# Optimization experiments

Hardware: AMD Instinct MI355X
Metric: run time of the kernel (lower is better)

Reference implementation:

```python
import jax, jax.numpy as jnp
import numpy as np

B, N = 2, 4096
SA, DG, ED, OUT = 128, 1024, 4, 128
RF = 0.1   # ED_radius_factor
EPS = 1e-5  # BatchNorm eps


def setup_inputs() -> dict:
    key = jax.random.key(0)
    ks = jax.random.split(key, 16)
    def w(k, sh, sc=0.05):
        return jax.random.normal(k, sh, jnp.float32) * sc
    return dict(
        pointcloud=jax.random.normal(ks[0], (B, N, 3), jnp.float32),
        h1=jax.random.normal(ks[1], (B, SA, N), jnp.float32),
        h2=jax.random.normal(ks[2], (B, DG, N), jnp.float32),
        dg_w1=w(ks[3], (256, DG)), dg_b1=jnp.zeros(256), dg_g1=jnp.ones(256), dg_be1=jnp.zeros(256),
        dg_w2=w(ks[4], (64, 256)), dg_b2=jnp.zeros(64), dg_g2=jnp.ones(64), dg_be2=jnp.zeros(64),
        dg_w3=w(ks[5], (32, 64)), dg_b3=jnp.zeros(32), dg_g3=jnp.ones(32), dg_be3=jnp.zeros(32),
        ed_w1=w(ks[6], (3, ED), 0.5), ed_b1=jnp.zeros(ED),
        ed_w2=w(ks[7], (ED, ED), 0.5), ed_b2=jnp.zeros(ED),
        w1=w(ks[8], (512, SA + 32 + ED)), b1=jnp.zeros(512), g1=jnp.ones(512), be1=jnp.zeros(512),
        w2=w(ks[9], (256, 512)), b2=jnp.zeros(256), g2=jnp.ones(256), be2=jnp.zeros(256),
        w3=w(ks[10], (OUT, 256)), b3=jnp.zeros(OUT), g3=jnp.ones(OUT), be3=jnp.zeros(OUT),
    )


def _conv1x1(x, w, b):  # x: (B,C,N) 1x1 Conv1d
    return jnp.einsum('oc,bcn->bon', w, x) + b[None, :, None]


def _bn(x, g, b):  # training-mode BatchNorm1d over (B,N) per channel
    m = x.mean(axis=(0, 2), keepdims=True)
    v = ((x - m) ** 2).mean(axis=(0, 2), keepdims=True)
    return g[None, :, None] * (x - m) * jax.lax.rsqrt(v + EPS) + b[None, :, None]


def _eigs(xyz):  # (N,3) -> (N,3) eigenvalues of per-point radius-neighbor covariance
    n = xyz.shape[0]
    x2 = (xyz * xyz).sum(-1)
    d2 = jnp.maximum(x2[:, None] + x2[None, :] - 2.0 * (xyz @ xyz.T), 0.0)
    dist = jnp.sqrt(jnp.maximum(d2, 1e-12))
    eye = jnp.eye(n, dtype=bool)
    max_d = jnp.where(eye, -jnp.inf, dist).max()  # calculate_distances max
    radius = max_d * RF                            # adaptive radius
    mask = ((dist < radius) & ~eye).astype(xyz.dtype)  # (N,N) radius neighbors, no self
    cnt = mask.sum(1)                              # true neighbor count (for the mean)
    mu = (mask @ xyz) / jnp.maximum(cnt, 1.0)[:, None]
    # sum_j m_ij x_j x_j^T via one matmul on flattened outer products
    S = (mask @ (xyz[:, :, None] * xyz[:, None, :]).reshape(n, 9)).reshape(n, 3, 3)
    # NOTE: original divides by k = mask.shape[0] == N (not neighbor count) -- kept faithfully
    cov = (S - cnt[:, None, None] * mu[:, :, None] * mu[:, None, :]) / n
    return jnp.linalg.eigvalsh(cov)


def reference(pointcloud, h1, h2,
              dg_w1, dg_b1, dg_g1, dg_be1,
              dg_w2, dg_b2, dg_g2, dg_be2,
              dg_w3, dg_b3, dg_g3, dg_be3,
              ed_w1, ed_b1, ed_w2, ed_b2,
              w1, b1, g1, be1, w2, b2, g2, be2, w3, b3, g3, be3):
    xyz = pointcloud[..., 0:3]
    # DG head: 1024 -> 256 -> 64 -> 32 (1x1 conv + BN + ReLU)
    f2 = jax.nn.relu(_bn(_conv1x1(h2, dg_w1, dg_b1), dg_g1, dg_be1))
    f2 = jax.nn.relu(_bn(_conv1x1(f2, dg_w2, dg_b2), dg_g2, dg_be2))
    f2 = jax.nn.relu(_bn(_conv1x1(f2, dg_w3, dg_b3), dg_g3, dg_be3))
    # ED branch: per-point local PCA eigenvalues + tiny MLP (3->4->4)
    eig = jax.vmap(_eigs)(xyz)                        # (B,N,3)
    h3 = jax.nn.relu(eig @ ed_w1 + ed_b1) @ ed_w2 + ed_b2  # (B,N,4)
    z = jnp.concatenate([h1, f2, jnp.transpose(h3, (0, 2, 1))], axis=1)  # (B,164,N)
    z = jax.nn.relu(_bn(_conv1x1(z, w1, b1), g1, be1))
    z = jax.nn.relu(_bn(_conv1x1(z, w2, b2), g2, be2))
    z = jax.nn.relu(_bn(_conv1x1(z, w3, b3), g3, be3))
    return (xyz, z)
```

## Files before the change

### kernel.cpp

```cpp
#include <hip/hip_runtime.h>
#include <math.h>

#define NPTS 4096
#define NB 2
#define BIGNEG -3.0e38f

typedef __attribute__((ext_vector_type(8))) short short8;
typedef __attribute__((ext_vector_type(4))) float f32x4;
typedef unsigned int uint32;

__device__ __forceinline__ unsigned short f2bf(float f) {
  uint32 u = __float_as_uint(f);
  uint32 r = (u + 0x7FFFu + ((u >> 16) & 1u)) >> 16;
  return (unsigned short)r;
}
__device__ __forceinline__ uint2 pack4(float a, float b, float c, float d) {
  uint2 r;
  r.x = (uint32)f2bf(a) | ((uint32)f2bf(b) << 16);
  r.y = (uint32)f2bf(c) | ((uint32)f2bf(d) << 16);
  return r;
}
__device__ __forceinline__ float bflo(uint32 w) { return __uint_as_float((w & 0xffffu) << 16); }
__device__ __forceinline__ float bfhi(uint32 w) { return __uint_as_float(w & 0xffff0000u); }

struct PrepP {
  const float *h2, *h1, *pc;
  const float* wsrc[6];
  unsigned short* wdst[6];
  unsigned short *h2t, *Zt;
  float *aZ, *bZ, *fZ, *f0;
  unsigned int* mx;
};

union ShPrep {
  float tile[64][65];
  struct { float4 sp[512]; float lm[8]; } m;
};

__global__ __launch_bounds__(256)
void prep_maxd2(PrepP P) {
  __shared__ ShPrep sh;
  int bid = blockIdx.x, tid = threadIdx.x;
  if (bid < 2304) {
    const float* src; unsigned short* dst; int S, C, b, c0, n0;
    if (bid < 2048) {
      b = bid >> 10; int r = bid & 1023;
      c0 = (r & 15) * 64; n0 = (r >> 4) * 64;
      src = P.h2; dst = P.h2t; S = 1024; C = 1024;
    } else {
      int r = bid - 2048; b = r >> 7; int r2 = r & 127;
      c0 = (r2 & 1) * 64; n0 = (r2 >> 1) * 64;
      src = P.h1; dst = P.Zt; S = 192; C = 128;
    }
    const float* sb = src + (size_t)b * C * NPTS;
#pragma unroll
    for (int p = 0; p < 4; ++p) {
      int r = (tid >> 4) + p * 16, q = tid & 15;
      float4 v = *(const float4*)(sb + (size_t)(c0 + r) * NPTS + n0 + q * 4);
      sh.tile[r][q * 4 + 0] = v.x;
      sh.tile[r][q * 4 + 1] = v.y;
      sh.tile[r][q * 4 + 2] = v.z;
      sh.tile[r][q * 4 + 3] = v.w;
    }
    __syncthreads();
#pragma unroll
    for (int p = 0; p < 2; ++p) {
      int n = (tid >> 3) + p * 32, j = tid & 7;
      uint2 lo = pack4(sh.tile[j * 8 + 0][n], sh.tile[j * 8 + 1][n], sh.tile[j * 8 + 2][n],
                       sh.tile[j * 8 + 3][n]);
      uint2 hi = pack4(sh.tile[j * 8 + 4][n], sh.tile[j * 8 + 5][n], sh.tile[j * 8 + 6][n],
                       sh.tile[j * 8 + 7][n]);
      *(uint4*)(dst + ((size_t)b * NPTS + n0 + n) * S + c0 + j * 8) =
          make_uint4(lo.x, lo.y, hi.x, hi.y);
    }
  } else if (bid < 2336) {
    int r = bid - 2304;
    for (int idx = r * 256 + tid; idx < NB * NPTS * 7; idx += 32 * 256) {
      int u = idx % 7, n = (idx / 7) & (NPTS - 1), b = idx / (7 * NPTS);
      *(uint2*)(P.Zt + ((size_t)b * NPTS + n) * 192 + 164 + u * 4) = make_uint2(0u, 0u);
    }
  } else if (bid < 2592) {
    const int segKp[6] = {1024, 256, 64, 192, 512, 256};
    const int segM[6] = {256, 64, 32, 512, 256, 128};
    const int segK[6] = {1024, 256, 64, 164, 512, 256};
    const int segEnd[6] = {262144, 278528, 282624, 380928, 512000, 544768};
    int r = bid - 2336;
    for (int idx = r * 256 + tid; idx < 544768; idx += 256 * 256) {
      int w = 0, start = 0;
#pragma unroll
      for (int s = 0; s < 6; ++s)
        if (idx >= segEnd[s]) { w = s + 1; start = segEnd[s]; }
      int local = idx - start, Kp = segKp[w], m = local / Kp, k = local % Kp;
      float v = (m < segM[w] && k < segK[w]) ? P.wsrc[w][m * segK[w] + k] : 0.f;
      P.wdst[w][local] = f2bf(v);
    }
  } else if (bid == 2592) {
    for (int ch = tid; ch < 512; ch += 256) {
      P.f0[ch] = 0.f;
      if (ch < 192) { P.aZ[ch] = 1.f; P.bZ[ch] = 0.f; P.fZ[ch] = BIGNEG; }
    }
  } else {
    int vb = bid - 2593;
    int b = vb >> 9, rem = vb & 511, it = rem & 63, jt = rem >> 6;
    int i0 = it * 64, j0 = jt * 512;
    const float* pb = P.pc + (size_t)b * NPTS * 3;
    for (int t = tid; t < 512; t += 256) {
      int j = j0 + t;
      float x = pb[j * 3], y = pb[j * 3 + 1], z = pb[j * 3 + 2];
      sh.m.sp[t] = make_float4(x, y, z, fmaf(x, x, fmaf(y, y, z * z)));
    }
    __syncthreads();
    int il = tid & 63, sl = tid >> 6;
    int i = i0 + il;
    float xi = pb[i * 3], yi = pb[i * 3 + 1], zi = pb[i * 3 + 2];
    float x2i = fmaf(xi, xi, fmaf(yi, yi, zi * zi));
    float m = 0.f;
#pragma unroll 4
    for (int j = sl * 128, e2 = sl * 128 + 128; j < e2; ++j) {
      float4 pj = sh.m.sp[j];
      float dot = fmaf(xi, pj.x, fmaf(yi, pj.y, zi * pj.z));
      m = fmaxf(m, fmaf(-2.f, dot, x2i + pj.w));
    }
#pragma unroll
    for (int off = 32; off > 0; off >>= 1) m = fmaxf(m, __shfl_xor(m, off, 64));
    if ((tid & 63) == 0) sh.m.lm[tid >> 6] = m;
    __syncthreads();
    if (tid == 0) {
      float v = fmaxf(fmaxf(sh.m.lm[0], sh.m.lm[1]), fmaxf(sh.m.lm[2], sh.m.lm[3]));
      atomicMax(&P.mx[b], __float_as_uint(v));
    }
  }
}

__global__ __launch_bounds__(256)
void eigs_partial(const float* __restrict__ pc, const unsigned int* __restrict__ mx,
                  float* __restrict__ part) {
  __shared__ float4 sp[1024];
  __shared__ float red[4][32][10];
  int b = blockIdx.z, js = blockIdx.y, it = blockIdx.x;
  int i0 = it * 32, j0 = js * 1024;
  int tid = threadIdx.x;
  const float* pb = pc + (size_t)b * NPTS * 3;
  for (int t = tid; t < 1024; t += 256) {
    int j = j0 + t;
    float x = pb[j * 3], y = pb[j * 3 + 1], z = pb[j * 3 + 2];
    sp[t] = make_float4(x, y, z, fmaf(x, x, fmaf(y, y, z * z)));
  }
  __syncthreads();
  int il = tid & 31, sl = tid >> 5;
  int i = i0 + il;
  float xi = pb[i * 3], yi = pb[i * 3 + 1], zi = pb[i * 3 + 2];
  float x2i = fmaf(xi, xi, fmaf(yi, yi, zi * zi));
  float r2 = 0.01f * fmaxf(__uint_as_float(mx[b]), 1e-12f);
  float v0 = 0, v1 = 0, v2 = 0, v3 = 0, v4 = 0, v5 = 0, v6 = 0, v7 = 0, v8 = 0, v9 = 0;
#pragma unroll 2
  for (int j = sl * 128, e2 = sl * 128 + 128; j < e2; ++j) {
    float4 pj = sp[j];
    float dot = fmaf(xi, pj.x, fmaf(yi, pj.y, zi * pj.z));
    float d2 = fmaf(-2.f, dot, x2i + pj.w);
    float msk = d2 < r2 ? 1.f : 0.f;
    float qx = msk * pj.x, qy = msk * pj.y, qz = msk * pj.z;
    v0 += msk; v1 += qx; v2 += qy; v3 += qz;
    v4 = fmaf(qx, pj.x, v4); v5 = fmaf(qx, pj.y, v5); v6 = fmaf(qx, pj.z, v6);
    v7 = fmaf(qy, pj.y, v7); v8 = fmaf(qy, pj.z, v8); v9 = fmaf(qz, pj.z, v9);
  }
  int iloc = i - j0;
  if (iloc >= sl * 128 && iloc < sl * 128 + 128) {
    v0 -= 1.f; v1 -= xi; v2 -= yi; v3 -= zi;
    v4 = fmaf(-xi, xi, v4); v5 = fmaf(-xi, yi, v5); v6 = fmaf(-xi, zi, v6);
    v7 = fmaf(-yi, yi, v7); v8 = fmaf(-yi, zi, v8); v9 = fmaf(-zi, zi, v9);
  }
  float vals[10] = {v0, v1, v2, v3, v4, v5, v6, v7, v8, v9};
#pragma unroll
  for (int v = 0; v < 10; ++v) vals[v] += __shfl_xor(vals[v], 32, 64);
  int w = tid >> 6;
  if ((tid & 63) < 32)
#pragma unroll
    for (int v = 0; v < 10; ++v) red[w][il][v] = vals[v];
  __syncthreads();
  if (tid < 32) {
    int ii = i0 + tid;
    size_t base = ((size_t)(b * 4 + js) * 10) * NPTS + ii;
#pragma unroll
    for (int v = 0; v < 10; ++v)
      part[base + (size_t)v * NPTS] =
          red[0][tid][v] + red[1][tid][v] + red[2][tid][v] + red[3][tid][v];
  }
}

struct GemmP {
  const unsigned short* Wp;
  const unsigned short* X;
  const float *aIn, *bIn, *fIn;
  unsigned short* Y;
  int Ystride;
  float *psum, *psq;
  int M, Kp;
};

template <int BN_IN>
__global__ __launch_bounds__(256)
void gemm_k(GemmP P) {
  __shared__ char db[2][18432];
  __shared__ float ash[512], bsh[512], fsh[512];
  const int tid = threadIdx.x;
  const int b = blockIdx.z, nt = blockIdx.x, mt = blockIdx.y;
  const int n0 = nt * 128, m0 = mt * 64;
  const int lane = tid & 63, wid = tid >> 6;
  const int wm = wid >> 1, wn = wid & 1, g = lane >> 4, c = lane & 15;
  const int kt = P.Kp >> 6;
  const unsigned short* Xb = P.X + (size_t)b * NPTS * P.Kp;

  if (BN_IN) {
    for (int ch = tid; ch < P.Kp; ch += 256) {
      ash[ch] = P.aIn[ch];
      bsh[ch] = P.bIn[ch];
      fsh[ch] = P.fIn[ch];
    }
    __syncthreads();
  }

  uint4 R0[4], R1[4];
  auto loadG = [&](int t, uint4* R) {
    int k0 = t << 6;
#pragma unroll
    for (int i = 0; i < 4; ++i) {
      int u = tid + i * 256, n = u >> 3, s = u & 7;
      R[i] = *(const uint4*)(Xb + (size_t)(n0 + n) * P.Kp + k0 + s * 8);
    }
  };
  auto writeS = [&](int buf, int t, uint4* R) {
    int k0 = t << 6;
#pragma unroll
    for (int i = 0; i < 4; ++i) {
      int u = tid + i * 256, s = u & 7;
      uint4 v = R[i];
      if (BN_IN) {
        int k = k0 + s * 8;
        float4 a0 = *(const float4*)&ash[k], a1 = *(const float4*)&ash[k + 4];
        float4 b0 = *(const float4*)&bsh[k], b1 = *(const float4*)&bsh[k + 4];
        float4 f0 = *(const float4*)&fsh[k], f1 = *(const float4*)&fsh[k + 4];
        uint2 lo = pack4(fmaxf(fmaf(bflo(v.x), a0.x, b0.x), f0.x),
                         fmaxf(fmaf(bfhi(v.x), a0.y, b0.y), f0.y),
                         fmaxf(fmaf(bflo(v.y), a0.z, b0.z), f0.z),
                         fmaxf(fmaf(bfhi(v.y), a0.w, b0.w), f0.w));
        uint2 hi = pack4(fmaxf(fmaf(bflo(v.z), a1.x, b1.x), f1.x),
                         fmaxf(fmaf(bfhi(v.z), a1.y, b1.y), f1.y),
                         fmaxf(fmaf(bflo(v.w), a1.z, b1.z), f1.z),
                         fmaxf(fmaf(bfhi(v.w), a1.w, b1.w), f1.w));
        v = make_uint4(lo.x, lo.y, hi.x, hi.y);
      }
      *(uint4*)&db[buf][(u >> 3) * 144 + (u & 7) * 16] = v;
    }
  };
  auto loadA = [&](int t, uint4* Af) {
    const unsigned short* base = P.Wp + (size_t)(m0 + wm * 32 + c) * P.Kp + (t << 6) + g * 8;
#pragma unroll
    for (int mf = 0; mf < 2; ++mf)
#pragma unroll
      for (int kw = 0; kw < 2; ++kw)
        Af[mf * 2 + kw] = *(const uint4*)(base + (size_t)mf * 16 * P.Kp + kw * 32);
  };

  f32x4 acc[2][4] = {};
  uint4 Acur[4], Anext[4] = {};
  loadG(0, R0);
  loadA(0, Acur);
  writeS(0, 0, R0);
  if (kt > 1) loadG(1, R1);
  __syncthreads();
  int cur = 0;

  auto step = [&](int t, uint4* Rload, uint4* Rwrite) {
    if (t + 2 < kt) loadG(t + 2, Rload);
    if (t + 1 < kt) loadA(t + 1, Anext);
#pragma unroll
    for (int kw = 0; kw < 2; ++kw) {
      union { uint4 u; short8 s; } a0, a1;
      a0.u = Acur[0 * 2 + kw];
      a1.u = Acur[1 * 2 + kw];
#pragma unroll
      for (int nf = 0; nf < 4; ++nf) {
        union { uint4 u; short8 s; } bf;
        bf.u = *(const uint4*)&db[cur][(wn * 64 + nf * 16 + c) * 144 + kw * 64 + g * 16];
        acc[0][nf] = __builtin_amdgcn_mfma_f32_16x16x32_bf16(a0.s, bf.s, acc[0][nf], 0, 0, 0);
        acc[1][nf] = __builtin_amdgcn_mfma_f32_16x16x32_bf16(a1.s, bf.s, acc[1][nf], 0, 0, 0);
      }
    }
    if (t + 1 < kt) writeS(cur ^ 1, t + 1, Rwrite);
    __syncthreads();
    cur ^= 1;
#pragma unroll
    for (int i = 0; i < 4; ++i) Acur[i] = Anext[i];
  };
  for (int t = 0; t < kt;) {
    step(t, R0, R1);
    ++t;
    if (t >= kt) break;
    step(t, R1, R0);
    ++t;
  }

#pragma unroll
  for (int nf = 0; nf < 4; ++nf) {
    int n = n0 + wn * 64 + nf * 16 + c;
    unsigned short* yrow = P.Y + ((size_t)b * NPTS + n) * P.Ystride;
#pragma unroll
    for (int mf = 0; mf < 2; ++mf) {
      int mb = m0 + wm * 32 + mf * 16 + g * 4;
      if (mb < P.M)
        *(uint2*)(yrow + mb) =
            pack4(acc[mf][nf][0], acc[mf][nf][1], acc[mf][nf][2], acc[mf][nf][3]);
    }
  }
  int slot = b * 64 + nt * 2 + wn;
#pragma unroll
  for (int mf = 0; mf < 2; ++mf)
#pragma unroll
    for (int r = 0; r < 4; ++r) {
      float s = 0.f, q = 0.f;
#pragma unroll
      for (int nf = 0; nf < 4; ++nf) {
        float v = acc[mf][nf][r];
        s += v;
        q = fmaf(v, v, q);
      }
#pragma unroll
      for (int m = 1; m < 16; m <<= 1) {
        s += __shfl_xor(s, m, 64);
        q += __shfl_xor(q, m, 64);
      }
      int row = m0 + wm * 32 + mf * 16 + g * 4 + r;
      if (c == 0 && row < P.M) {
        P.psum[(size_t)row * 128 + slot] = s;
        P.psq[(size_t)row * 128 + slot] = q;
      }
    }
}

__global__ __launch_bounds__(128)
void bn_finalize(const float* __restrict__ psum, const float* __restrict__ psq,
                 const float* __restrict__ gamma, const float* __restrict__ beta,
                 float* __restrict__ a_, float* __restrict__ b_, float* __restrict__ f_) {
  int ch = blockIdx.x, t = threadIdx.x;
  float s = psum[(size_t)ch * 128 + t];
  float q = psq[(size_t)ch * 128 + t];
#pragma unroll
  for (int m = 1; m < 64; m <<= 1) {
    s += __shfl_xor(s, m, 64);
    q += __shfl_xor(q, m, 64);
  }
  __shared__ float ws[2][2];
  if ((t & 63) == 0) { ws[t >> 6][0] = s; ws[t >> 6][1] = q; }
  __syncthreads();
  if (t == 0) {
    float S = ws[0][0] + ws[1][0];
    float Q = ws[0][1] + ws[1][1];
    const float inv = 1.f / (float)(NB * NPTS);
    float mean = S * inv;
    float var = fmaxf(Q * inv - mean * mean, 0.f);
    float aa = rsqrtf(var + 1e-5f) * gamma[ch];
    a_[ch] = aa;
    b_[ch] = beta[ch] - mean * aa;
    if (f_) f_[ch] = 0.f;
  }
}

__global__ __launch_bounds__(256)
void eigs_finalize(const float* __restrict__ part, const float* __restrict__ ew1,
                   const float* __restrict__ eb1, const float* __restrict__ ew2,
                   const float* __restrict__ eb2, unsigned short* __restrict__ Zt) {
  int p = blockIdx.x * 256 + threadIdx.x;
  int b = p >> 12, i = p & (NPTS - 1);
  float t[10];
#pragma unroll
  for (int v = 0; v < 10; ++v) {
    float s = 0.f;
#pragma unroll
    for (int js = 0; js < 4; ++js) s += part[((size_t)(b * 4 + js) * 10 + v) * NPTS + i];
    t[v] = s;
  }
  double cntd = (double)t[0];
  double denom = cntd > 1.0 ? cntd : 1.0;
  double mux = t[1] / denom, muy = t[2] / denom, muz = t[3] / denom;
  const double inv_n = 1.0 / (double)NPTS;
  double a00 = ((double)t[4] - cntd * mux * mux) * inv_n;
  double a01 = ((double)t[5] - cntd * mux * muy) * inv_n;
  double a02 = ((double)t[6] - cntd * mux * muz) * inv_n;
  double a11 = ((double)t[7] - cntd * muy * muy) * inv_n;
  double a12 = ((double)t[8] - cntd * muy * muz) * inv_n;
  double a22 = ((double)t[9] - cntd * muz * muz) * inv_n;
  double e0, e1, e2;
  double p1 = a01 * a01 + a02 * a02 + a12 * a12;
  double q = (a00 + a11 + a22) / 3.0;
  double d0 = a00 - q, d1 = a11 - q, d2q = a22 - q;
  double p2 = d0 * d0 + d1 * d1 + d2q * d2q + 2.0 * p1;
  if (p2 <= 1e-30) {
    e0 = e1 = e2 = q;
  } else {
    double pp = sqrt(p2 / 6.0);
    double ip = 1.0 / pp;
    double b00 = d0 * ip, b11 = d1 * ip, b22 = d2q * ip;
    double b01 = a01 * ip, b02 = a02 * ip, b12 = a12 * ip;
    double detB = b00 * (b11 * b22 - b12 * b12) - b01 * (b01 * b22 - b12 * b02) +
                  b02 * (b01 * b12 - b11 * b02);
    double r = detB * 0.5;
    r = r < -1.0 ? -1.0 : (r > 1.0 ? 1.0 : r);
    double phi = acos(r) / 3.0;
    e2 = q + 2.0 * pp * cos(phi);
    e0 = q + 2.0 * pp * cos(phi + 2.0943951023931953);
    e1 = 3.0 * q - e0 - e2;
  }
  float eg[3] = {(float)e0, (float)e1, (float)e2};
  float tmp[4];
#pragma unroll
  for (int e = 0; e < 4; ++e) {
    float v = eb1[e];
#pragma unroll
    for (int k = 0; k < 3; ++k) v = fmaf(eg[k], ew1[k * 4 + e], v);
    tmp[e] = fmaxf(v, 0.f);
  }
  float h3[4];
#pragma unroll
  for (int f = 0; f < 4; ++f) {
    float v = eb2[f];
#pragma unroll
    for (int e = 0; e < 4; ++e) v = fmaf(tmp[e], ew2[e * 4 + f], v);
    h3[f] = v;
  }
  *(uint2*)(Zt + ((size_t)b * NPTS + i) * 192 + 160) = pack4(h3[0], h3[1], h3[2], h3[3]);
}

__global__ __launch_bounds__(256)
void out_final(const unsigned short* __restrict__ Y, const float* __restrict__ a_,
               const float* __restrict__ b_, const float* __restrict__ pc,
               float* __restrict__ out) {
  int bid = blockIdx.x;
  if (bid < 1024) {
    __shared__ float tile[32][33];
    int b = bid >> 9, r0 = bid & 511;
    int c0 = (r0 & 3) * 32, n0 = (r0 >> 2) * 32;
    int r = threadIdx.x >> 3, q = threadIdx.x & 7;
    uint2 v = *(const uint2*)(Y + ((size_t)b * NPTS + n0 + r) * 128 + c0 + q * 4);
    float4 aa = *(const float4*)(a_ + c0 + q * 4);
    float4 bb = *(const float4*)(b_ + c0 + q * 4);
    tile[r][q * 4 + 0] = fmaxf(bflo(v.x) * aa.x + bb.x, 0.f);
    tile[r][q * 4 + 1] = fmaxf(bfhi(v.x) * aa.y + bb.y, 0.f);
    tile[r][q * 4 + 2] = fmaxf(bflo(v.y) * aa.z + bb.z, 0.f);
    tile[r][q * 4 + 3] = fmaxf(bfhi(v.y) * aa.w + bb.w, 0.f);
    __syncthreads();
    float4 o = make_float4(tile[q * 4 + 0][r], tile[q * 4 + 1][r], tile[q * 4 + 2][r],
                           tile[q * 4 + 3][r]);
    float* z = out + (size_t)NB * NPTS * 3;
    *(float4*)(z + ((size_t)b * 128 + c0 + r) * NPTS + n0 + q * 4) = o;
  } else {
    int i = (bid - 1024) * 256 + threadIdx.x;
    ((float4*)out)[i] = ((const float4*)pc)[i];
  }
}

extern "C" void kernel_launch(void* const* d_in, const int* in_sizes, int n_in,
                              void* d_out, int out_size, void* d_ws, size_t ws_size,
                              hipStream_t stream) {
  (void)in_sizes; (void)n_in; (void)out_size; (void)ws_size;
  const float* pc    = (const float*)d_in[0];
  const float* h1    = (const float*)d_in[1];
  const float* h2    = (const float*)d_in[2];
  const float* dgw1  = (const float*)d_in[3];
  const float* dgg1  = (const float*)d_in[5];
  const float* dgbe1 = (const float*)d_in[6];
  const float* dgw2  = (const float*)d_in[7];
  const float* dgg2  = (const float*)d_in[9];
  const float* dgbe2 = (const float*)d_in[10];
  const float* dgw3  = (const float*)d_in[11];
  const float* dgg3  = (const float*)d_in[13];
  const float* dgbe3 = (const float*)d_in[14];
  const float* ew1   = (const float*)d_in[15];
  const float* eb1   = (const float*)d_in[16];
  const float* ew2   = (const float*)d_in[17];
  const float* eb2   = (const float*)d_in[18];
  const float* w1    = (const float*)d_in[19];
  const float* g1    = (const float*)d_in[21];
  const float* be1   = (const float*)d_in[22];
  const float* w2    = (const float*)d_in[23];
  const float* g2    = (const float*)d_in[25];
  const float* be2   = (const float*)d_in[26];
  const float* w3    = (const float*)d_in[27];
  const float* g3    = (const float*)d_in[29];
  const float* be3   = (const float*)d_in[30];
  float* out = (float*)d_out;

  char* p = (char*)d_ws;
  auto take = [&](size_t bytes) { char* r = p; p += (bytes + 255) & ~(size_t)255; return r; };
  unsigned int* mx = (unsigned int*)take(64);
  unsigned short* h2t = (unsigned short*)take((size_t)NB * NPTS * 1024 * 2);
  unsigned short* Zt  = (unsigned short*)take((size_t)NB * NPTS * 192 * 2);
  unsigned short* wp1 = (unsigned short*)take((size_t)256 * 1024 * 2);
  unsigned short* wp2 = (unsigned short*)take((size_t)64 * 256 * 2);
  unsigned short* wp3 = (unsigned short*)take((size_t)64 * 64 * 2);
  unsigned short* wp4 = (unsigned short*)take((size_t)512 * 192 * 2);
  unsigned short* wp5 = (unsigned short*)take((size_t)256 * 512 * 2);
  unsigned short* wp6 = (unsigned short*)take((size_t)128 * 256 * 2);
  unsigned short* yA  = (unsigned short*)take((size_t)NB * NPTS * 256 * 2);
  unsigned short* yB  = (unsigned short*)take((size_t)NB * NPTS * 512 * 2);
  float* psum = (float*)take((size_t)512 * 128 * 4);
  float* psq  = (float*)take((size_t)512 * 128 * 4);
  float* a1 = (float*)take(512 * 4); float* b1 = (float*)take(512 * 4);
  float* a2 = (float*)take(512 * 4); float* b2 = (float*)take(512 * 4);
  float* aZ = (float*)take(512 * 4); float* bZ = (float*)take(512 * 4);
  float* fZ = (float*)take(512 * 4);
  float* a4 = (float*)take(512 * 4); float* b4 = (float*)take(512 * 4);
  float* a5 = (float*)take(512 * 4); float* b5 = (float*)take(512 * 4);
  float* a6 = (float*)take(512 * 4); float* b6 = (float*)take(512 * 4);
  float* f0 = (float*)take(512 * 4);
  float* part = (float*)take((size_t)NB * 4 * 10 * NPTS * 4);

  hipMemsetAsync(mx, 0, 64, stream);

  PrepP PP;
  PP.h2 = h2; PP.h1 = h1; PP.pc = pc;
  PP.wsrc[0] = dgw1; PP.wsrc[1] = dgw2; PP.wsrc[2] = dgw3;
  PP.wsrc[3] = w1;   PP.wsrc[4] = w2;   PP.wsrc[5] = w3;
  PP.wdst[0] = wp1; PP.wdst[1] = wp2; PP.wdst[2] = wp3;
  PP.wdst[3] = wp4; PP.wdst[4] = wp5; PP.wdst[5] = wp6;
  PP.h2t = h2t; PP.Zt = Zt;
  PP.aZ = aZ; PP.bZ = bZ; PP.fZ = fZ; PP.f0 = f0;
  PP.mx = mx;
  prep_maxd2<<<3617, 256, 0, stream>>>(PP);

  eigs_partial<<<dim3(NPTS / 32, 4, NB), 256, 0, stream>>>(pc, mx, part);
  eigs_finalize<<<NB * NPTS / 256, 256, 0, stream>>>(part, ew1, eb1, ew2, eb2, Zt);

  GemmP L1 = {wp1, h2t, nullptr, nullptr, nullptr, yA, 256, psum, psq, 256, 1024};
  gemm_k<0><<<dim3(32, 4, NB), 256, 0, stream>>>(L1);
  bn_finalize<<<256, 128, 0, stream>>>(psum, psq, dgg1, dgbe1, a1, b1, nullptr);

  GemmP L2 = {wp2, yA, a1, b1, f0, yB, 64, psum, psq, 64, 256};
  gemm_k<1><<<dim3(32, 1, NB), 256, 0, stream>>>(L2);
  bn_finalize<<<64, 128, 0, stream>>>(psum, psq, dgg2, dgbe2, a2, b2, nullptr);

  GemmP L3 = {wp3, yB, a2, b2, f0, Zt + 128, 192, psum, psq, 32, 64};
  gemm_k<1><<<dim3(32, 1, NB), 256, 0, stream>>>(L3);
  bn_finalize<<<32, 128, 0, stream>>>(psum, psq, dgg3, dgbe3, aZ + 128, bZ + 128, fZ + 128);

  GemmP L4 = {wp4, Zt, aZ, bZ, fZ, yB, 512, psum, psq, 512, 192};
  gemm_k<1><<<dim3(32, 8, NB), 256, 0, stream>>>(L4);
  bn_finalize<<<512, 128, 0, stream>>>(psum, psq, g1, be1, a4, b4, nullptr);

  GemmP L5 = {wp5, yB, a4, b4, f0, yA, 256, psum, psq, 256, 512};
  gemm_k<1><<<dim3(32, 4, NB), 256, 0, stream>>>(L5);
  bn_finalize<<<256, 128, 0, stream>>>(psum, psq, g2, be2, a5, b5, nullptr);

  GemmP L6 = {wp6, yA, a5, b5, f0, yB, 128, psum, psq, 128, 256};
  gemm_k<1><<<dim3(32, 2, NB), 256, 0, stream>>>(L6);
  bn_finalize<<<128, 128, 0, stream>>>(psum, psq, g3, be3, a6, b6, nullptr);

  out_final<<<1048, 256, 0, stream>>>(yB, a6, b6, pc, out);
}
```

Before: 148.3 us.

## Fold eigen-partial and eigen-finalize kernels into extra blocks of DG GEMM launches

Removes the two standalone eigenvalue kernels and runs their work as extra grid blocks appended to the first and second DG-head GEMM launches, selected by blockIdx.z. Shared memory becomes a union so both roles fit in one allocation. The aim is to save two kernel launches and let the small, latency-bound eigen work overlap with the GEMMs that fill the GPU poorly. In exchange the GEMM kernel carries more code and registers, and the union's larger shared footprint could reduce occupancy for the plain GEMM launches.

```diff
diff --git a/kernel.cpp b/kernel.cpp
--- a/kernel.cpp
+++ b/kernel.cpp
@@ -132,62 +132,6 @@
   }
 }
 
-__global__ __launch_bounds__(256)
-void eigs_partial(const float* __restrict__ pc, const unsigned int* __restrict__ mx,
-                  float* __restrict__ part) {
-  __shared__ float4 sp[1024];
-  __shared__ float red[4][32][10];
-  int b = blockIdx.z, js = blockIdx.y, it = blockIdx.x;
-  int i0 = it * 32, j0 = js * 1024;
-  int tid = threadIdx.x;
-  const float* pb = pc + (size_t)b * NPTS * 3;
-  for (int t = tid; t < 1024; t += 256) {
-    int j = j0 + t;
-    float x = pb[j * 3], y = pb[j * 3 + 1], z = pb[j * 3 + 2];
-    sp[t] = make_float4(x, y, z, fmaf(x, x, fmaf(y, y, z * z)));
-  }
-  __syncthreads();
-  int il = tid & 31, sl = tid >> 5;
-  int i = i0 + il;
-  float xi = pb[i * 3], yi = pb[i * 3 + 1], zi = pb[i * 3 + 2];
-  float x2i = fmaf(xi, xi, fmaf(yi, yi, zi * zi));
-  float r2 = 0.01f * fmaxf(__uint_as_float(mx[b]), 1e-12f);
-  float v0 = 0, v1 = 0, v2 = 0, v3 = 0, v4 = 0, v5 = 0, v6 = 0, v7 = 0, v8 = 0, v9 = 0;
-#pragma unroll 2
-  for (int j = sl * 128, e2 = sl * 128 + 128; j < e2; ++j) {
-    float4 pj = sp[j];
-    float dot = fmaf(xi, pj.x, fmaf(yi, pj.y, zi * pj.z));
-    float d2 = fmaf(-2.f, dot, x2i + pj.w);
-    float msk = d2 < r2 ? 1.f : 0.f;
-    float qx = msk * pj.x, qy = msk * pj.y, qz = msk * pj.z;
-    v0 += msk; v1 += qx; v2 += qy; v3 += qz;
-    v4 = fmaf(qx, pj.x, v4); v5 = fmaf(qx, pj.y, v5); v6 = fmaf(qx, pj.z, v6);
-    v7 = fmaf(qy, pj.y, v7); v8 = fmaf(qy, pj.z, v8); v9 = fmaf(qz, pj.z, v9);
-  }
-  int iloc = i - j0;
-  if (iloc >= sl * 128 && iloc < sl * 128 + 128) {
-    v0 -= 1.f; v1 -= xi; v2 -= yi; v3 -= zi;
-    v4 = fmaf(-xi, xi, v4); v5 = fmaf(-xi, yi, v5); v6 = fmaf(-xi, zi, v6);
-    v7 = fmaf(-yi, yi, v7); v8 = fmaf(-yi, zi, v8); v9 = fmaf(-zi, zi, v9);
-  }
-  float vals[10] = {v0, v1, v2, v3, v4, v5, v6, v7, v8, v9};
-#pragma unroll
-  for (int v = 0; v < 10; ++v) vals[v] += __shfl_xor(vals[v], 32, 64);
-  int w = tid >> 6;
-  if ((tid & 63) < 32)
-#pragma unroll
-    for (int v = 0; v < 10; ++v) red[w][il][v] = vals[v];
-  __syncthreads();
-  if (tid < 32) {
-    int ii = i0 + tid;
-    size_t base = ((size_t)(b * 4 + js) * 10) * NPTS + ii;
-#pragma unroll
-    for (int v = 0; v < 10; ++v)
-      part[base + (size_t)v * NPTS] =
-          red[0][tid][v] + red[1][tid][v] + red[2][tid][v] + red[3][tid][v];
-  }
-}
-
 struct GemmP {
   const unsigned short* Wp;
   const unsigned short* X;
@@ -197,13 +141,143 @@
   float *psum, *psq;
   int M, Kp;
 };
-
-template <int BN_IN>
+struct EigP {
+  const float* pc;
+  const unsigned int* mx;
+  float* part;
+  const float *ew1, *eb1, *ew2, *eb2;
+  unsigned short* Zt;
+};
+
+union ShG {
+  struct { char db[2][18432]; float ash[512], bsh[512], fsh[512]; } g;
+  struct { float4 sp[1024]; float red[4][32][10]; } e;
+};
+
+template <int BN_IN, int EIG>
 __global__ __launch_bounds__(256)
-void gemm_k(GemmP P) {
-  __shared__ char db[2][18432];
-  __shared__ float ash[512], bsh[512], fsh[512];
+void gemm_k(GemmP P, EigP E) {
+  __shared__ ShG sh;
   const int tid = threadIdx.x;
+
+  if (EIG == 1 && blockIdx.z >= NB) {
+    int e = blockIdx.x + 32 * blockIdx.y + 128 * (blockIdx.z - NB);
+    int b = e >> 9, rem = e & 511, it = rem & 127, js = rem >> 7;
+    int i0 = it * 32, j0 = js * 1024;
+    const float* pb = E.pc + (size_t)b * NPTS * 3;
+    for (int t = tid; t < 1024; t += 256) {
+      int j = j0 + t;
+      float x = pb[j * 3], y = pb[j * 3 + 1], z = pb[j * 3 + 2];
+      sh.e.sp[t] = make_float4(x, y, z, fmaf(x, x, fmaf(y, y, z * z)));
+    }
+    __syncthreads();
+    int il = tid & 31, sl = tid >> 5;
+    int i = i0 + il;
+    float xi = pb[i * 3], yi = pb[i * 3 + 1], zi = pb[i * 3 + 2];
+    float x2i = fmaf(xi, xi, fmaf(yi, yi, zi * zi));
+    float r2 = 0.01f * fmaxf(__uint_as_float(E.mx[b]), 1e-12f);
+    float v0 = 0, v1 = 0, v2 = 0, v3 = 0, v4 = 0, v5 = 0, v6 = 0, v7 = 0, v8 = 0, v9 = 0;
+#pragma unroll 2
+    for (int j = sl * 128, e2 = sl * 128 + 128; j < e2; ++j) {
+      float4 pj = sh.e.sp[j];
+      float dot = fmaf(xi, pj.x, fmaf(yi, pj.y, zi * pj.z));
+      float d2 = fmaf(-2.f, dot, x2i + pj.w);
+      float msk = d2 < r2 ? 1.f : 0.f;
+      float qx = msk * pj.x, qy = msk * pj.y, qz = msk * pj.z;
+      v0 += msk; v1 += qx; v2 += qy; v3 += qz;
+      v4 = fmaf(qx, pj.x, v4); v5 = fmaf(qx, pj.y, v5); v6 = fmaf(qx, pj.z, v6);
+      v7 = fmaf(qy, pj.y, v7); v8 = fmaf(qy, pj.z, v8); v9 = fmaf(qz, pj.z, v9);
+    }
+    int iloc = i - j0;
+    if (iloc >= sl * 128 && iloc < sl * 128 + 128) {
+      v0 -= 1.f; v1 -= xi; v2 -= yi; v3 -= zi;
+      v4 = fmaf(-xi, xi, v4); v5 = fmaf(-xi, yi, v5); v6 = fmaf(-xi, zi, v6);
+      v7 = fmaf(-yi, yi, v7); v8 = fmaf(-yi, zi, v8); v9 = fmaf(-zi, zi, v9);
+    }
+    float vals[10] = {v0, v1, v2, v3, v4, v5, v6, v7, v8, v9};
+#pragma unroll
+    for (int v = 0; v < 10; ++v) vals[v] += __shfl_xor(vals[v], 32, 64);
+    int w = tid >> 6;
+    if ((tid & 63) < 32)
+#pragma unroll
+      for (int v = 0; v < 10; ++v) sh.e.red[w][il][v] = vals[v];
+    __syncthreads();
+    if (tid < 32) {
+      int ii = i0 + tid;
+      size_t base = ((size_t)(b * 4 + js) * 10) * NPTS + ii;
+#pragma unroll
+      for (int v = 0; v < 10; ++v)
+        E.part[base + (size_t)v * NPTS] =
+            sh.e.red[0][tid][v] + sh.e.red[1][tid][v] + sh.e.red[2][tid][v] +
+            sh.e.red[3][tid][v];
+    }
+    return;
+  }
+
+  if (EIG == 2 && blockIdx.z >= NB) {
+    int p = blockIdx.x * 256 + tid;
+    int b = p >> 12, i = p & (NPTS - 1);
+    float t[10];
+#pragma unroll
+    for (int v = 0; v < 10; ++v) {
+      float s = 0.f;
+#pragma unroll
+      for (int js = 0; js < 4; ++js)
+        s += E.part[((size_t)(b * 4 + js) * 10 + v) * NPTS + i];
+      t[v] = s;
+    }
+    double cntd = (double)t[0];
+    double denom = cntd > 1.0 ? cntd : 1.0;
+    double mux = t[1] / denom, muy = t[2] / denom, muz = t[3] / denom;
+    const double inv_n = 1.0 / (double)NPTS;
+    double a00 = ((double)t[4] - cntd * mux * mux) * inv_n;
+    double a01 = ((double)t[5] - cntd * mux * muy) * inv_n;
+    double a02 = ((double)t[6] - cntd * mux * muz) * inv_n;
+    double a11 = ((double)t[7] - cntd * muy * muy) * inv_n;
+    double a12 = ((double)t[8] - cntd * muy * muz) * inv_n;
+    double a22 = ((double)t[9] - cntd * muz * muz) * inv_n;
+    double e0, e1, e2;
+    double p1 = a01 * a01 + a02 * a02 + a12 * a12;
+    double q = (a00 + a11 + a22) / 3.0;
+    double d0 = a00 - q, d1 = a11 - q, d2q = a22 - q;
+    double p2 = d0 * d0 + d1 * d1 + d2q * d2q + 2.0 * p1;
+    if (p2 <= 1e-30) {
+      e0 = e1 = e2 = q;
+    } else {
+      double pp = sqrt(p2 / 6.0);
+      double ip = 1.0 / pp;
+      double b00 = d0 * ip, b11 = d1 * ip, b22 = d2q * ip;
+      double b01 = a01 * ip, b02 = a02 * ip, b12 = a12 * ip;
+      double detB = b00 * (b11 * b22 - b12 * b12) - b01 * (b01 * b22 - b12 * b02) +
+                    b02 * (b01 * b12 - b11 * b02);
+      double r = detB * 0.5;
+      r = r < -1.0 ? -1.0 : (r > 1.0 ? 1.0 : r);
+      double phi = acos(r) / 3.0;
+      e2 = q + 2.0 * pp * cos(phi);
+      e0 = q + 2.0 * pp * cos(phi + 2.0943951023931953);
+      e1 = 3.0 * q - e0 - e2;
+    }
+    float eg[3] = {(float)e0, (float)e1, (float)e2};
+    float tmp[4];
+#pragma unroll
+    for (int e = 0; e < 4; ++e) {
+      float v = E.eb1[e];
+#pragma unroll
+      for (int k = 0; k < 3; ++k) v = fmaf(eg[k], E.ew1[k * 4 + e], v);
+      tmp[e] = fmaxf(v, 0.f);
+    }
+    float h3[4];
+#pragma unroll
+    for (int f = 0; f < 4; ++f) {
+      float v = E.eb2[f];
+#pragma unroll
+      for (int e = 0; e < 4; ++e) v = fmaf(tmp[e], E.ew2[e * 4 + f], v);
+      h3[f] = v;
+    }
+    *(uint2*)(E.Zt + ((size_t)b * NPTS + i) * 192 + 160) = pack4(h3[0], h3[1], h3[2], h3[3]);
+    return;
+  }
+
   const int b = blockIdx.z, nt = blockIdx.x, mt = blockIdx.y;
   const int n0 = nt * 128, m0 = mt * 64;
   const int lane = tid & 63, wid = tid >> 6;
@@ -213,9 +287,9 @@
 
   if (BN_IN) {
     for (int ch = tid; ch < P.Kp; ch += 256) {
-      ash[ch] = P.aIn[ch];
-      bsh[ch] = P.bIn[ch];
-      fsh[ch] = P.fIn[ch];
+      sh.g.ash[ch] = P.aIn[ch];
+      sh.g.bsh[ch] = P.bIn[ch];
+      sh.g.fsh[ch] = P.fIn[ch];
     }
     __syncthreads();
   }
@@ -237,9 +311,9 @@
       uint4 v = R[i];
       if (BN_IN) {
         int k = k0 + s * 8;
-        float4 a0 = *(const float4*)&ash[k], a1 = *(const float4*)&ash[k + 4];
-        float4 b0 = *(const float4*)&bsh[k], b1 = *(const float4*)&bsh[k + 4];
-        float4 f0 = *(const float4*)&fsh[k], f1 = *(const float4*)&fsh[k + 4];
+        float4 a0 = *(const float4*)&sh.g.ash[k], a1 = *(const float4*)&sh.g.ash[k + 4];
+        float4 b0 = *(const float4*)&sh.g.bsh[k], b1 = *(const float4*)&sh.g.bsh[k + 4];
+        float4 f0 = *(const float4*)&sh.g.fsh[k], f1 = *(const float4*)&sh.g.fsh[k + 4];
         uint2 lo = pack4(fmaxf(fmaf(bflo(v.x), a0.x, b0.x), f0.x),
                          fmaxf(fmaf(bfhi(v.x), a0.y, b0.y), f0.y),
                          fmaxf(fmaf(bflo(v.y), a0.z, b0.z), f0.z),
@@ -250,7 +324,7 @@
                          fmaxf(fmaf(bfhi(v.w), a1.w, b1.w), f1.w));
         v = make_uint4(lo.x, lo.y, hi.x, hi.y);
       }
-      *(uint4*)&db[buf][(u >> 3) * 144 + (u & 7) * 16] = v;
+      *(uint4*)&sh.g.db[buf][(u >> 3) * 144 + (u & 7) * 16] = v;
     }
   };
   auto loadA = [&](int t, uint4* Af) {
@@ -282,7 +356,7 @@
 #pragma unroll
       for (int nf = 0; nf < 4; ++nf) {
         union { uint4 u; short8 s; } bf;
-        bf.u = *(const uint4*)&db[cur][(wn * 64 + nf * 16 + c) * 144 + kw * 64 + g * 16];
+        bf.u = *(const uint4*)&sh.g.db[cur][(wn * 64 + nf * 16 + c) * 144 + kw * 64 + g * 16];
         acc[0][nf] = __builtin_amdgcn_mfma_f32_16x16x32_bf16(a0.s, bf.s, acc[0][nf], 0, 0, 0);
         acc[1][nf] = __builtin_amdgcn_mfma_f32_16x16x32_bf16(a1.s, bf.s, acc[1][nf], 0, 0, 0);
       }
@@ -364,71 +438,6 @@
     b_[ch] = beta[ch] - mean * aa;
     if (f_) f_[ch] = 0.f;
   }
-}
-
-__global__ __launch_bounds__(256)
-void eigs_finalize(const float* __restrict__ part, const float* __restrict__ ew1,
-                   const float* __restrict__ eb1, const float* __restrict__ ew2,
-                   const float* __restrict__ eb2, unsigned short* __restrict__ Zt) {
-  int p = blockIdx.x * 256 + threadIdx.x;
-  int b = p >> 12, i = p & (NPTS - 1);
-  float t[10];
-#pragma unroll
-  for (int v = 0; v < 10; ++v) {
-    float s = 0.f;
-#pragma unroll
-    for (int js = 0; js < 4; ++js) s += part[((size_t)(b * 4 + js) * 10 + v) * NPTS + i];
-    t[v] = s;
-  }
-  double cntd = (double)t[0];
-  double denom = cntd > 1.0 ? cntd : 1.0;
-  double mux = t[1] / denom, muy = t[2] / denom, muz = t[3] / denom;
-  const double inv_n = 1.0 / (double)NPTS;
-  double a00 = ((double)t[4] - cntd * mux * mux) * inv_n;
-  double a01 = ((double)t[5] - cntd * mux * muy) * inv_n;
-  double a02 = ((double)t[6] - cntd * mux * muz) * inv_n;
-  double a11 = ((double)t[7] - cntd * muy * muy) * inv_n;
-  double a12 = ((double)t[8] - cntd * muy * muz) * inv_n;
-  double a22 = ((double)t[9] - cntd * muz * muz) * inv_n;
-  double e0, e1, e2;
-  double p1 = a01 * a01 + a02 * a02 + a12 * a12;
-  double q = (a00 + a11 + a22) / 3.0;
-  double d0 = a00 - q, d1 = a11 - q, d2q = a22 - q;
-  double p2 = d0 * d0 + d1 * d1 + d2q * d2q + 2.0 * p1;
-  if (p2 <= 1e-30) {
-    e0 = e1 = e2 = q;
-  } else {
-    double pp = sqrt(p2 / 6.0);
-    double ip = 1.0 / pp;
-    double b00 = d0 * ip, b11 = d1 * ip, b22 = d2q * ip;
-    double b01 = a01 * ip, b02 = a02 * ip, b12 = a12 * ip;
-    double detB = b00 * (b11 * b22 - b12 * b12) - b01 * (b01 * b22 - b12 * b02) +
-                  b02 * (b01 * b12 - b11 * b02);
-    double r = detB * 0.5;
-    r = r < -1.0 ? -1.0 : (r > 1.0 ? 1.0 : r);
-    double phi = acos(r) / 3.0;
-    e2 = q + 2.0 * pp * cos(phi);
-    e0 = q + 2.0 * pp * cos(phi + 2.0943951023931953);
-    e1 = 3.0 * q - e0 - e2;
-  }
-  float eg[3] = {(float)e0, (float)e1, (float)e2};
-  float tmp[4];
-#pragma unroll
-  for (int e = 0; e < 4; ++e) {
-    float v = eb1[e];
-#pragma unroll
-    for (int k = 0; k < 3; ++k) v = fmaf(eg[k], ew1[k * 4 + e], v);
-    tmp[e] = fmaxf(v, 0.f);
-  }
-  float h3[4];
-#pragma unroll
-  for (int f = 0; f < 4; ++f) {
-    float v = eb2[f];
-#pragma unroll
-    for (int e = 0; e < 4; ++e) v = fmaf(tmp[e], ew2[e * 4 + f], v);
-    h3[f] = v;
-  }
-  *(uint2*)(Zt + ((size_t)b * NPTS + i) * 192 + 160) = pack4(h3[0], h3[1], h3[2], h3[3]);
 }
 
 __global__ __launch_bounds__(256)
@@ -528,31 +537,30 @@
   PP.mx = mx;
   prep_maxd2<<<3617, 256, 0, stream>>>(PP);
 
-  eigs_partial<<<dim3(NPTS / 32, 4, NB), 256, 0, stream>>>(pc, mx, part);
-  eigs_finalize<<<NB * NPTS / 256, 256, 0, stream>>>(part, ew1, eb1, ew2, eb2, Zt);
+  EigP EP = {pc, mx, part, ew1, eb1, ew2, eb2, Zt};
 
   GemmP L1 = {wp1, h2t, nullptr, nullptr, nullptr, yA, 256, psum, psq, 256, 1024};
-  gemm_k<0><<<dim3(32, 4, NB), 256, 0, stream>>>(L1);
+  gemm_k<0, 1><<<dim3(32, 4, NB + 8), 256, 0, stream>>>(L1, EP);
   bn_finalize<<<256, 128, 0, stream>>>(psum, psq, dgg1, dgbe1, a1, b1, nullptr);
 
   GemmP L2 = {wp2, yA, a1, b1, f0, yB, 64, psum, psq, 64, 256};
-  gemm_k<1><<<dim3(32, 1, NB), 256, 0, stream>>>(L2);
+  gemm_k<1, 2><<<dim3(32, 1, NB + 1), 256, 0, stream>>>(L2, EP);
   bn_finalize<<<64, 128, 0, stream>>>(psum, psq, dgg2, dgbe2, a2, b2, nullptr);
 
   GemmP L3 = {wp3, yB, a2, b2, f0, Zt + 128, 192, psum, psq, 32, 64};
-  gemm_k<1><<<dim3(32, 1, NB), 256, 0, stream>>>(L3);
+  gemm_k<1, 0><<<dim3(32, 1, NB), 256, 0, stream>>>(L3, EP);
   bn_finalize<<<32, 128, 0, stream>>>(psum, psq, dgg3, dgbe3, aZ + 128, bZ + 128, fZ + 128);
 
   GemmP L4 = {wp4, Zt, aZ, bZ, fZ, yB, 512, psum, psq, 512, 192};
-  gemm_k<1><<<dim3(32, 8, NB), 256, 0, stream>>>(L4);
+  gemm_k<1, 0><<<dim3(32, 8, NB), 256, 0, stream>>>(L4, EP);
   bn_finalize<<<512, 128, 0, stream>>>(psum, psq, g1, be1, a4, b4, nullptr);
 
   GemmP L5 = {wp5, yB, a4, b4, f0, yA, 256, psum, psq, 256, 512};
-  gemm_k<1><<<dim3(32, 4, NB), 256, 0, stream>>>(L5);
+  gemm_k<1, 0><<<dim3(32, 4, NB), 256, 0, stream>>>(L5, EP);
   bn_finalize<<<256, 128, 0, stream>>>(psum, psq, g2, be2, a5, b5, nullptr);
 
   GemmP L6 = {wp6, yA, a5, b5, f0, yB, 128, psum, psq, 128, 256};
-  gemm_k<1><<<dim3(32, 2, NB), 256, 0, stream>>>(L6);
+  gemm_k<1, 0><<<dim3(32, 2, NB), 256, 0, stream>>>(L6, EP);
   bn_finalize<<<128, 128, 0, stream>>>(psum, psq, g3, be3, a6, b6, nullptr);
 
   out_final<<<1048, 256, 0, stream>>>(yB, a6, b6, pc, out);
```

New measurement: 142.3 us. -4.1%, faster.
